# Optimization experiments

Hardware: AMD Instinct MI355X
Metric: run time of the kernel (lower is better)

## Reference

```python
import jax, jax.numpy as jnp
import numpy as np

N_NODES = 50000
N_EDGES = 500000
D = 128
BN_EPS = 1e-5


def setup_inputs() -> dict:
    key = jax.random.key(0)
    ks = jax.random.split(key, 6)
    x = jax.random.normal(ks[0], (N_NODES, D), dtype=jnp.float32)
    edge_attr = jax.random.normal(ks[1], (N_EDGES, D), dtype=jnp.float32)
    edge_source = jax.random.randint(ks[2], (N_EDGES,), 0, N_NODES, dtype=jnp.int32)
    edge_target = jax.random.randint(ks[3], (N_EDGES,), 0, N_NODES, dtype=jnp.int32)
    # Linear weights stored as [in, out] = [3*D, D]; scaled like torch default init
    scale = 1.0 / np.sqrt(3 * D)
    Wf = jax.random.normal(ks[4], (3 * D, D), dtype=jnp.float32) * scale
    Ws = jax.random.normal(ks[5], (3 * D, D), dtype=jnp.float32) * scale
    bf = jnp.zeros((D,), dtype=jnp.float32)
    bs = jnp.zeros((D,), dtype=jnp.float32)
    gamma = jnp.ones((D,), dtype=jnp.float32)
    beta = jnp.zeros((D,), dtype=jnp.float32)
    return {"x": x, "edge_attr": edge_attr, "edge_source": edge_source,
            "edge_target": edge_target, "Wf": Wf, "bf": bf, "Ws": Ws, "bs": bs,
            "gamma": gamma, "beta": beta}


def reference(x, edge_attr, edge_source, edge_target, Wf, bf, Ws, bs, gamma, beta):
    # gather + concat: z is [E, 3*D]
    z = jnp.concatenate([x[edge_source], x[edge_target], edge_attr], axis=-1)
    # gated edge messages: sigmoid(linear_f(z)) * softplus(linear_s(z))  [E, D]
    msg = jax.nn.sigmoid(z @ Wf + bf) * jax.nn.softplus(z @ Ws + bs)
    # scatter-sum back to source nodes  [N, D]
    agg = jax.ops.segment_sum(msg, edge_source, num_segments=N_NODES)
    # BatchNorm1d (training mode: batch stats, biased variance)
    mean = jnp.mean(agg, axis=0)
    var = jnp.var(agg, axis=0)
    agg_bn = (agg - mean) * jax.lax.rsqrt(var + BN_EPS) * gamma + beta
    return jax.nn.softplus(x + agg_bn)
```

## Files before the change

### kernel.cpp

```cpp
#include <hip/hip_runtime.h>
#include <math.h>
#include <stdint.h>

#define N_NODES 50000
#define N_EDGES 500000
#define D 128
#define BE 128
#define NKT 6
#define WROW 72
#define MROW 136
#define LOG2E 1.4426950408889634f
#define LN2   0.6931471805599453f

typedef __attribute__((ext_vector_type(8))) short bf16x8;
typedef __attribute__((ext_vector_type(4))) float floatx4;

__device__ __forceinline__ float fast_sigmoid(float v) {
    return __builtin_amdgcn_rcpf(1.0f + __builtin_amdgcn_exp2f(-v * LOG2E));
}
__device__ __forceinline__ float fast_softplus(float v) {
    float t = __builtin_amdgcn_exp2f(-fabsf(v) * LOG2E);
    return fmaxf(v, 0.0f) + __builtin_amdgcn_logf(1.0f + t) * LN2;
}
__device__ __forceinline__ uint32_t pack_bf16(float a, float b) {
    union { float f; uint32_t u; } ca, cb; ca.f = a; cb.f = b;
    return __builtin_amdgcn_perm(cb.u + 0x8000u, ca.u + 0x8000u, 0x07060302);
}
__device__ __forceinline__ unsigned short f2bf(float f) {
    union { float f; uint32_t u; } c; c.f = f;
    return (unsigned short)((c.u + 0x8000u) >> 16);
}

__global__ __launch_bounds__(256) void wt_prepass(
    const float* __restrict__ Wf, const float* __restrict__ Ws,
    unsigned short* __restrict__ Wt)
{
    const int kt = blockIdx.x >> 3;
    const int i  = blockIdx.x & 7;
    const int n  = threadIdx.x;
    const float* src = (n < 128) ? (Wf + n) : (Ws + (n - 128));
    const int k0 = kt * 64 + i * 8;
    uint32_t u[4];
#pragma unroll
    for (int j = 0; j < 4; j++) {
        float a = src[(size_t)(k0 + 2 * j) * D];
        float b = src[(size_t)(k0 + 2 * j + 1) * D];
        u[j] = pack_bf16(a, b);
    }
    uint4 v; v.x = u[0]; v.y = u[1]; v.z = u[2]; v.w = u[3];
    *(uint4*)(Wt + (size_t)(kt * 256 + n) * WROW + i * 8) = v;
}

__global__ __launch_bounds__(512, 4) void edge_msg_mfma(
    const float* __restrict__ x, const float* __restrict__ edge_attr,
    const int* __restrict__ esrc, const int* __restrict__ etgt,
    const unsigned short* __restrict__ Wt,
    const float* __restrict__ bfp, const float* __restrict__ bsp,
    float* __restrict__ agg, unsigned short* __restrict__ msgs,
    int* __restrict__ cnt, int mode)
{
    __shared__ unsigned short sW[256 * WROW];
    __shared__ unsigned short sZ[BE * WROW];
    __shared__ int sSrc[BE];
    __shared__ int sTgt[BE];

    const int tid  = threadIdx.x;
    const int lane = tid & 63;
    const int w    = tid >> 6;
    const int wc   = w & 3;
    const int wr   = w >> 2;
    const int e0   = blockIdx.x * BE;

    if (tid < BE) {
        sSrc[tid] = (e0 + tid < N_EDGES) ? esrc[e0 + tid] : 0;
    } else if (tid < 2 * BE) {
        int m = tid - BE;
        sTgt[m] = (e0 + m < N_EDGES) ? etgt[e0 + m] : 0;
    }
    __syncthreads();

    floatx4 acc[4][4];
#pragma unroll
    for (int mt = 0; mt < 4; mt++)
#pragma unroll
        for (int nt = 0; nt < 4; nt++) {
            floatx4 z = {0.f, 0.f, 0.f, 0.f};
            acc[mt][nt] = z;
        }

    const int zm = tid >> 2;
    const int zk = (tid & 3) * 16;

#pragma unroll 1
    for (int kt = 0; kt < NKT; kt++) {
        {
            const char* gbase = (const char*)Wt + (size_t)kt * 36864 + lane * 16;
            char* lbase = (char*)sW;
#pragma unroll
            for (int i = 0; i < 5; i++) {
                int c = w + i * 8;
                if (c < 36) {
                    __builtin_amdgcn_global_load_lds(
                        (const __attribute__((address_space(1))) void*)(gbase + c * 1024),
                        (__attribute__((address_space(3))) void*)(lbase + c * 1024),
                        16, 0, 0);
                }
            }
        }
        {
            const float* zsrc;
            int half = (kt & 1) * 64;
            if (kt < 2)      zsrc = x + (size_t)sSrc[zm] * D + half;
            else if (kt < 4) zsrc = x + (size_t)sTgt[zm] * D + half;
            else {
                int eg = e0 + zm;
                zsrc = edge_attr + (size_t)(eg < N_EDGES ? eg : 0) * D + half;
            }
            float4 f0 = *(const float4*)(zsrc + zk);
            float4 f1 = *(const float4*)(zsrc + zk + 4);
            float4 f2 = *(const float4*)(zsrc + zk + 8);
            float4 f3 = *(const float4*)(zsrc + zk + 12);
            uint4 lo, hi;
            lo.x = pack_bf16(f0.x, f0.y); lo.y = pack_bf16(f0.z, f0.w);
            lo.z = pack_bf16(f1.x, f1.y); lo.w = pack_bf16(f1.z, f1.w);
            hi.x = pack_bf16(f2.x, f2.y); hi.y = pack_bf16(f2.z, f2.w);
            hi.z = pack_bf16(f3.x, f3.y); hi.w = pack_bf16(f3.z, f3.w);
            uint32_t* dz = (uint32_t*)(sZ + (size_t)zm * WROW) + (zk >> 1);
            *(uint4*)(dz)     = lo;
            *(uint4*)(dz + 4) = hi;
        }
        __syncthreads();

#pragma unroll
        for (int ks = 0; ks < 2; ks++) {
            const int kb = ks * 32 + (lane >> 4) * 8;
            bf16x8 afr[4];
#pragma unroll
            for (int mt = 0; mt < 4; mt++)
                afr[mt] = *(const bf16x8*)(sZ + (wr * 64 + mt * 16 + (lane & 15)) * WROW + kb);
            bf16x8 bfr[4];
#pragma unroll
            for (int nt = 0; nt < 4; nt++) {
                int n = (nt < 2) ? (wc * 32 + nt * 16 + (lane & 15))
                                 : (128 + wc * 32 + (nt - 2) * 16 + (lane & 15));
                bfr[nt] = *(const bf16x8*)(sW + n * WROW + kb);
            }
#pragma unroll
            for (int mt = 0; mt < 4; mt++)
#pragma unroll
                for (int nt = 0; nt < 4; nt++)
                    acc[mt][nt] = __builtin_amdgcn_mfma_f32_16x16x32_bf16(
                        afr[mt], bfr[nt], acc[mt][nt], 0, 0, 0);
        }
        __syncthreads();
    }

    if (mode) {
        unsigned short* sM = sW;
#pragma unroll
        for (int nt = 0; nt < 2; nt++) {
            const int col = wc * 32 + nt * 16 + (lane & 15);
            const float bF = bfp[col];
            const float bS = bsp[col];
#pragma unroll
            for (int mt = 0; mt < 4; mt++) {
#pragma unroll
                for (int r = 0; r < 4; r++) {
                    int mm = wr * 64 + mt * 16 + (lane >> 4) * 4 + r;
                    float f = acc[mt][nt][r] + bF;
                    float s = acc[mt][nt + 2][r] + bS;
                    sM[mm * MROW + col] = f2bf(fast_sigmoid(f) * fast_softplus(s));
                }
            }
        }
        __syncthreads();
        {
            const int r = tid >> 2;
            const int c = tid & 3;
            if (e0 + r < N_EDGES) {
                const uint4* sp = (const uint4*)(sM + r * MROW + c * 32);
                uint4 v0 = sp[0], v1 = sp[1], v2 = sp[2], v3 = sp[3];
                uint4* dp = (uint4*)(msgs + (size_t)(e0 + r) * D + c * 32);
                dp[0] = v0; dp[1] = v1; dp[2] = v2; dp[3] = v3;
            }
        }
        if (tid < BE && e0 + tid < N_EDGES) atomicAdd(&cnt[sSrc[tid]], 1);
    } else {
#pragma unroll
        for (int nt = 0; nt < 2; nt++) {
            const int col = wc * 32 + nt * 16 + (lane & 15);
            const float bF = bfp[col];
            const float bS = bsp[col];
#pragma unroll
            for (int mt = 0; mt < 4; mt++) {
#pragma unroll
                for (int r = 0; r < 4; r++) {
                    int mm = wr * 64 + mt * 16 + (lane >> 4) * 4 + r;
                    int eg = e0 + mm;
                    if (eg >= N_EDGES) continue;
                    float f = acc[mt][nt][r] + bF;
                    float s = acc[mt][nt + 2][r] + bS;
                    atomicAdd(agg + (size_t)sSrc[mm] * D + col,
                              fast_sigmoid(f) * fast_softplus(s));
                }
            }
        }
    }
}

__global__ __launch_bounds__(1024) void scan1_kernel(
    const int* __restrict__ cnt, int* __restrict__ ofs, int* __restrict__ bsum)
{
    __shared__ int sh[1024];
    const int t = threadIdx.x;
    const int n = blockIdx.x * 1024 + t;
    int c = (n < N_NODES) ? cnt[n] : 0;
    sh[t] = c;
    __syncthreads();
    for (int off = 1; off < 1024; off <<= 1) {
        int v = (t >= off) ? sh[t - off] : 0;
        __syncthreads();
        sh[t] += v;
        __syncthreads();
    }
    if (n < N_NODES) ofs[n] = sh[t] - c;
    if (t == 1023) bsum[blockIdx.x] = sh[1023];
}

__global__ __launch_bounds__(64) void scan2_kernel(int* __restrict__ bsum)
{
    if (threadIdx.x == 0) {
        int v[49];
#pragma unroll
        for (int i = 0; i < 49; i++) v[i] = bsum[i];
        int run = 0;
#pragma unroll
        for (int i = 0; i < 49; i++) { bsum[i] = run; run += v[i]; }
    }
}

__global__ __launch_bounds__(512) void fill_kernel(
    const int* __restrict__ esrc, int* __restrict__ ofs,
    const int* __restrict__ bsum, int* __restrict__ eidx)
{
    int e = blockIdx.x * 512 + threadIdx.x;
    if (e < N_EDGES) {
        int s = esrc[e];
        int slot = atomicAdd(&ofs[s], 1) + bsum[s >> 10];
        eidx[slot] = e;
    }
}

__global__ __launch_bounds__(256) void gather_kernel(
    const unsigned short* __restrict__ msgs, const int* __restrict__ eidx,
    const int* __restrict__ cnt, const int* __restrict__ ofs,
    const int* __restrict__ bsum, float* __restrict__ agg)
{
    __shared__ float red[2][64][2];
    const int tid  = threadIdx.x;
    const int lane = tid & 63;
    const int w2   = (tid >> 6) & 1;
    const int h    = tid >> 7;
    const int n    = blockIdx.x * 2 + h;
    const int deg  = cnt[n];
    const int base = bsum[n >> 10] + ofs[n] - deg;
    float a0 = 0.0f, a1 = 0.0f;
    for (int j = w2; j < deg; j += 2) {
        int id = eidx[base + j];
        uint32_t p = *(const uint32_t*)(msgs + (size_t)id * D + 2 * lane);
        union { uint32_t u; float f; } c0, c1;
        c0.u = p << 16;
        c1.u = p & 0xFFFF0000u;
        a0 += c0.f; a1 += c1.f;
    }
    if (w2 == 1) { red[h][lane][0] = a0; red[h][lane][1] = a1; }
    __syncthreads();
    if (w2 == 0) {
        a0 += red[h][lane][0];
        a1 += red[h][lane][1];
        float2 o; o.x = a0; o.y = a1;
        *(float2*)(agg + (size_t)n * D + 2 * lane) = o;
    }
}

#define STATS_BLOCKS 128
__global__ __launch_bounds__(256) void bn_stats_kernel(
    const float* __restrict__ agg, float* __restrict__ stats)
{
    __shared__ float4 redS[256];
    __shared__ float4 redQ[256];
    const int c4 = threadIdx.x & 31;
    const int rg = threadIdx.x >> 5;
    const int rows = (N_NODES + STATS_BLOCKS - 1) / STATS_BLOCKS;
    const int r0 = blockIdx.x * rows;
    const int r1 = min(r0 + rows, N_NODES);
    const float4* a4 = (const float4*)agg;

    float4 s = {0, 0, 0, 0}, q = {0, 0, 0, 0};
    for (int r = r0 + rg; r < r1; r += 8) {
        float4 v = a4[(size_t)r * 32 + c4];
        s.x += v.x; s.y += v.y; s.z += v.z; s.w += v.w;
        q.x += v.x * v.x; q.y += v.y * v.y; q.z += v.z * v.z; q.w += v.w * v.w;
    }
    redS[threadIdx.x] = s;
    redQ[threadIdx.x] = q;
    __syncthreads();
    if (rg == 0) {
#pragma unroll
        for (int j = 1; j < 8; j++) {
            float4 ts = redS[c4 + j * 32], tq = redQ[c4 + j * 32];
            s.x += ts.x; s.y += ts.y; s.z += ts.z; s.w += ts.w;
            q.x += tq.x; q.y += tq.y; q.z += tq.z; q.w += tq.w;
        }
        atomicAdd(&stats[c4 * 4 + 0], s.x);
        atomicAdd(&stats[c4 * 4 + 1], s.y);
        atomicAdd(&stats[c4 * 4 + 2], s.z);
        atomicAdd(&stats[c4 * 4 + 3], s.w);
        atomicAdd(&stats[D + c4 * 4 + 0], q.x);
        atomicAdd(&stats[D + c4 * 4 + 1], q.y);
        atomicAdd(&stats[D + c4 * 4 + 2], q.z);
        atomicAdd(&stats[D + c4 * 4 + 3], q.w);
    }
}

__global__ __launch_bounds__(256) void bn_final_kernel(
    const float* __restrict__ x, const float* __restrict__ agg,
    const float* __restrict__ stats,
    const float* __restrict__ gamma, const float* __restrict__ beta,
    float* __restrict__ out)
{
    const int idx = blockIdx.x * blockDim.x + threadIdx.x;
    const int total4 = N_NODES * D / 4;
    if (idx >= total4) return;
    const int c4 = idx & (D / 4 - 1);
    const float inv_n = 1.0f / (float)N_NODES;

    float4 sm = *(const float4*)&stats[c4 * 4];
    float4 sq = *(const float4*)&stats[D + c4 * 4];
    float4 g  = *(const float4*)&gamma[c4 * 4];
    float4 b  = *(const float4*)&beta[c4 * 4];
    float4 xv = ((const float4*)x)[idx];
    float4 av = ((const float4*)agg)[idx];

    float4 o;
    {
        float mean = sm.x * inv_n, var = sq.x * inv_n - mean * mean;
        float is = rsqrtf(var + 1e-5f) * g.x;
        o.x = fast_softplus(xv.x + (av.x - mean) * is + b.x);
    }
    {
        float mean = sm.y * inv_n, var = sq.y * inv_n - mean * mean;
        float is = rsqrtf(var + 1e-5f) * g.y;
        o.y = fast_softplus(xv.y + (av.y - mean) * is + b.y);
    }
    {
        float mean = sm.z * inv_n, var = sq.z * inv_n - mean * mean;
        float is = rsqrtf(var + 1e-5f) * g.z;
        o.z = fast_softplus(xv.z + (av.z - mean) * is + b.z);
    }
    {
        float mean = sm.w * inv_n, var = sq.w * inv_n - mean * mean;
        float is = rsqrtf(var + 1e-5f) * g.w;
        o.w = fast_softplus(xv.w + (av.w - mean) * is + b.w);
    }
    ((float4*)out)[idx] = o;
}

extern "C" void kernel_launch(void* const* d_in, const int* in_sizes, int n_in,
                              void* d_out, int out_size, void* d_ws, size_t ws_size,
                              hipStream_t stream) {
    const float* x         = (const float*)d_in[0];
    const float* edge_attr = (const float*)d_in[1];
    const int*   esrc      = (const int*)d_in[2];
    const int*   etgt      = (const int*)d_in[3];
    const float* Wf        = (const float*)d_in[4];
    const float* bf_       = (const float*)d_in[5];
    const float* Ws        = (const float*)d_in[6];
    const float* bs_       = (const float*)d_in[7];
    const float* gamma     = (const float*)d_in[8];
    const float* beta      = (const float*)d_in[9];
    float* out = (float*)d_out;

    float* agg   = (float*)d_ws;
    float* stats = agg + (size_t)N_NODES * D;
    int*   cnt   = (int*)(stats + 2 * D);
    int*   ofs   = cnt + N_NODES;
    int*   bsum  = ofs + N_NODES;
    unsigned short* Wt = (unsigned short*)(bsum + 256);
    int*   eidx  = (int*)((char*)Wt + 221184);
    unsigned short* msgs = (unsigned short*)(eidx + N_EDGES);
    const size_t NEED = 25600000ULL + 1024 + 200000 + 200000 + 1024
                      + 221184 + 2000000 + 128000000ULL;
    const int mode = (ws_size >= NEED) ? 1 : 0;

    wt_prepass<<<48, 256, 0, stream>>>(Wf, Ws, Wt);
    if (mode) {
        hipMemsetAsync(stats, 0, 1024 + 200000, stream);
        edge_msg_mfma<<<(N_EDGES + BE - 1) / BE, 512, 0, stream>>>(
            x, edge_attr, esrc, etgt, Wt, bf_, bs_, agg, msgs, cnt, 1);
        scan1_kernel<<<49, 1024, 0, stream>>>(cnt, ofs, bsum);
        scan2_kernel<<<1, 64, 0, stream>>>(bsum);
        fill_kernel<<<(N_EDGES + 511) / 512, 512, 0, stream>>>(esrc, ofs, bsum, eidx);
        gather_kernel<<<N_NODES / 2, 256, 0, stream>>>(msgs, eidx, cnt, ofs, bsum, agg);
    } else {
        hipMemsetAsync(d_ws, 0, ((size_t)N_NODES * D + 2 * D) * sizeof(float), stream);
        edge_msg_mfma<<<(N_EDGES + BE - 1) / BE, 512, 0, stream>>>(
            x, edge_attr, esrc, etgt, Wt, bf_, bs_, agg, msgs, cnt, 0);
    }
    bn_stats_kernel<<<STATS_BLOCKS, 256, 0, stream>>>(agg, stats);
    bn_final_kernel<<<(N_NODES * D / 4 + 255) / 256, 256, 0, stream>>>(
        x, agg, stats, gamma, beta, out);
}
```

Measured before the change: 649.2 us.

## Double-buffer weight slabs in LDS and prefetch gathered Z rows into registers

The K loop now keeps two LDS slabs for the weights. While the current slab is consumed by MFMA, the next slab is loaded asynchronously with global_load_lds, and the next K step's gathered x/edge_attr rows are loaded into registers. The trailing barrier becomes a bare s_barrier, and launch bounds drop from 4 to 2 blocks' worth of waves. The aim is to hide gather and weight-load latency behind matrix work. The cost is roughly doubled weight LDS per block, which likely cuts resident blocks per CU and the latency hiding that occupancy gave.

```diff
diff --git a/kernel.cpp b/kernel.cpp
--- a/kernel.cpp
+++ b/kernel.cpp
@@ -8,6 +8,7 @@
 #define BE 128
 #define NKT 6
 #define WROW 72
+#define WSLAB (256 * WROW)
 #define MROW 136
 #define LOG2E 1.4426950408889634f
 #define LN2   0.6931471805599453f
@@ -51,7 +52,7 @@
     *(uint4*)(Wt + (size_t)(kt * 256 + n) * WROW + i * 8) = v;
 }
 
-__global__ __launch_bounds__(512, 4) void edge_msg_mfma(
+__global__ __launch_bounds__(512, 2) void edge_msg_mfma(
     const float* __restrict__ x, const float* __restrict__ edge_attr,
     const int* __restrict__ esrc, const int* __restrict__ etgt,
     const unsigned short* __restrict__ Wt,
@@ -59,7 +60,7 @@
     float* __restrict__ agg, unsigned short* __restrict__ msgs,
     int* __restrict__ cnt, int mode)
 {
-    __shared__ unsigned short sW[256 * WROW];
+    __shared__ unsigned short sW[2 * WSLAB];
     __shared__ unsigned short sZ[BE * WROW];
     __shared__ int sSrc[BE];
     __shared__ int sTgt[BE];
@@ -91,46 +92,60 @@
     const int zm = tid >> 2;
     const int zk = (tid & 3) * 16;
 
+    float4 zr0, zr1, zr2, zr3;
+
+    auto issue_w = [&](int kt, int slab) {
+        const char* gbase = (const char*)Wt + (size_t)kt * 36864 + lane * 16;
+        char* lbase = (char*)sW + slab * 36864;
+#pragma unroll
+        for (int i = 0; i < 5; i++) {
+            int c = w + i * 8;
+            if (c < 36) {
+                __builtin_amdgcn_global_load_lds(
+                    (const __attribute__((address_space(1))) void*)(gbase + c * 1024),
+                    (__attribute__((address_space(3))) void*)(lbase + c * 1024),
+                    16, 0, 0);
+            }
+        }
+    };
+    auto issue_z = [&](int kt) {
+        const float* zsrc;
+        int half = (kt & 1) * 64;
+        if (kt < 2)      zsrc = x + (size_t)sSrc[zm] * D + half;
+        else if (kt < 4) zsrc = x + (size_t)sTgt[zm] * D + half;
+        else {
+            int eg = e0 + zm;
+            zsrc = edge_attr + (size_t)(eg < N_EDGES ? eg : 0) * D + half;
+        }
+        zr0 = *(const float4*)(zsrc + zk);
+        zr1 = *(const float4*)(zsrc + zk + 4);
+        zr2 = *(const float4*)(zsrc + zk + 8);
+        zr3 = *(const float4*)(zsrc + zk + 12);
+    };
+
+    issue_w(0, 0);
+    issue_z(0);
+
 #pragma unroll 1
     for (int kt = 0; kt < NKT; kt++) {
         {
-            const char* gbase = (const char*)Wt + (size_t)kt * 36864 + lane * 16;
-            char* lbase = (char*)sW;
-#pragma unroll
-            for (int i = 0; i < 5; i++) {
-                int c = w + i * 8;
-                if (c < 36) {
-                    __builtin_amdgcn_global_load_lds(
-                        (const __attribute__((address_space(1))) void*)(gbase + c * 1024),
-                        (__attribute__((address_space(3))) void*)(lbase + c * 1024),
-                        16, 0, 0);
-                }
-            }
-        }
-        {
-            const float* zsrc;
-            int half = (kt & 1) * 64;
-            if (kt < 2)      zsrc = x + (size_t)sSrc[zm] * D + half;
-            else if (kt < 4) zsrc = x + (size_t)sTgt[zm] * D + half;
-            else {
-                int eg = e0 + zm;
-                zsrc = edge_attr + (size_t)(eg < N_EDGES ? eg : 0) * D + half;
-            }
-            float4 f0 = *(const float4*)(zsrc + zk);
-            float4 f1 = *(const float4*)(zsrc + zk + 4);
-            float4 f2 = *(const float4*)(zsrc + zk + 8);
-            float4 f3 = *(const float4*)(zsrc + zk + 12);
             uint4 lo, hi;
-            lo.x = pack_bf16(f0.x, f0.y); lo.y = pack_bf16(f0.z, f0.w);
-            lo.z = pack_bf16(f1.x, f1.y); lo.w = pack_bf16(f1.z, f1.w);
-            hi.x = pack_bf16(f2.x, f2.y); hi.y = pack_bf16(f2.z, f2.w);
-            hi.z = pack_bf16(f3.x, f3.y); hi.w = pack_bf16(f3.z, f3.w);
+            lo.x = pack_bf16(zr0.x, zr0.y); lo.y = pack_bf16(zr0.z, zr0.w);
+            lo.z = pack_bf16(zr1.x, zr1.y); lo.w = pack_bf16(zr1.z, zr1.w);
+            hi.x = pack_bf16(zr2.x, zr2.y); hi.y = pack_bf16(zr2.z, zr2.w);
+            hi.z = pack_bf16(zr3.x, zr3.y); hi.w = pack_bf16(zr3.z, zr3.w);
             uint32_t* dz = (uint32_t*)(sZ + (size_t)zm * WROW) + (zk >> 1);
             *(uint4*)(dz)     = lo;
             *(uint4*)(dz + 4) = hi;
         }
         __syncthreads();
 
+        if (kt + 1 < NKT) {
+            issue_w(kt + 1, (kt + 1) & 1);
+            issue_z(kt + 1);
+        }
+
+        const unsigned short* sWb = sW + (kt & 1) * WSLAB;
 #pragma unroll
         for (int ks = 0; ks < 2; ks++) {
             const int kb = ks * 32 + (lane >> 4) * 8;
@@ -143,7 +158,7 @@
             for (int nt = 0; nt < 4; nt++) {
                 int n = (nt < 2) ? (wc * 32 + nt * 16 + (lane & 15))
                                  : (128 + wc * 32 + (nt - 2) * 16 + (lane & 15));
-                bfr[nt] = *(const bf16x8*)(sW + n * WROW + kb);
+                bfr[nt] = *(const bf16x8*)(sWb + n * WROW + kb);
             }
 #pragma unroll
             for (int mt = 0; mt < 4; mt++)
@@ -152,7 +167,7 @@
                     acc[mt][nt] = __builtin_amdgcn_mfma_f32_16x16x32_bf16(
                         afr[mt], bfr[nt], acc[mt][nt], 0, 0, 0);
         }
-        __syncthreads();
+        __builtin_amdgcn_s_barrier();
     }
 
     if (mode) {
```

New measurement: 730.1 us. 12.5% more time.
